# Kernel tuning notes

Measured on AMD Instinct MI355X. Metric: run time of the kernel, lower is better.

The kernel has to match this reference:

```python
import jax, jax.numpy as jnp
import numpy as np
from jax import lax

STRIDES = (8, 16, 32)
NUM_CLASSES = 80
TOPK = 1000
CONF_THRESH = 0.05
NMS_THRESH = 0.6


def setup_inputs() -> dict:
    key = jax.random.key(0)
    ks = jax.random.split(key, 10)
    hw = [(256, 256), (128, 128), (64, 64)]
    inp = {}
    for lv, (h, w) in enumerate(hw):
        inp[f"cls_pred_{lv}"] = jax.random.normal(ks[3 * lv + 0], (NUM_CLASSES, h, w), jnp.float32)
        inp[f"reg_pred_{lv}"] = jax.random.normal(ks[3 * lv + 1], (4, h, w), jnp.float32)
        inp[f"ctn_pred_{lv}"] = jax.random.normal(ks[3 * lv + 2], (1, h, w), jnp.float32)
    inp["scales"] = jax.random.uniform(ks[9], (3,), jnp.float32)
    return inp


def _level_decode(cls_p, reg_p, ctn_p, scale, stride):
    # cls_p: [C,H,W] -> flatten to [M,C] matching torch permute(1,2,0).view(-1,C)
    C, H, W = cls_p.shape
    cls = jnp.transpose(cls_p, (1, 2, 0)).reshape(-1, C)          # [M,C]
    reg = jnp.transpose(reg_p, (1, 2, 0)).reshape(-1, 4)          # [M,4]
    reg = jax.nn.relu(reg * scale) * stride                       # Scale + relu + stride
    ctn = jnp.transpose(ctn_p, (1, 2, 0)).reshape(-1, 1)          # [M,1]
    joint = jnp.sqrt(jax.nn.sigmooid(cls) * jax.nn.sigmoid(ctn)) if False else \
        jnp.sqrt(jax.nn.sigmoid(cls) * jax.nn.sigmoid(ctn))      # [M,C]
    scores = jnp.max(joint, axis=-1)                              # [M]
    labels = jnp.argmax(joint, axis=-1)                           # [M]
    ay, ax = jnp.meshgrid(jnp.arange(H), jnp.arange(W), indexing='ij')
    anchors = (jnp.stack([ax, ay], -1).reshape(-1, 2).astype(cls.dtype) + 0.5) * stride  # [M,2]
    # per-level topk (M > TOPK for all levels here)
    scores, idx = lax.top_k(scores, TOPK)
    labels = labels[idx]
    reg = reg[idx]
    anchors = anchors[idx]
    boxes = jnp.concatenate([anchors - reg[:, :2], anchors + reg[:, 2:]], axis=-1)  # x1y1x2y2
    return scores, labels, boxes


def _nms(boxes, scores):
    # Faithful port of the pure-python NMS: fixed-shape keep mask, sorted order.
    N = boxes.shape[0]
    order = jnp.argsort(-scores)
    b = boxes[order]
    x1, y1, x2, y2 = b[:, 0], b[:, 1], b[:, 2], b[:, 3]
    areas = (x2 - x1) * (y2 - y1)
    xx1 = jnp.maximum(x1[:, None], x1[None, :])
    yy1 = jnp.maximum(y1[:, None], y1[None, :])
    xx2 = jnp.minimum(x2[:, None], x2[None, :])
    yy2 = jnp.minimum(y2[:, None], y2[None, :])
    w = jnp.maximum(1e-10, xx2 - xx1)
    h = jnp.maximum(1e-10, yy2 - yy1)
    inter = w * h
    iou = inter / (areas[:, None] + areas[None, :] - inter + 1e-14)  # [N,N]
    idxs = jnp.arange(N)

    def body(i, keep):
        sup = (iou[i] > NMS_THRESH) & (idxs > i) & keep[i]
        return keep & ~sup

    keep = lax.fori_loop(0, N, body, jnp.ones((N,), bool))
    return order, keep


def reference(cls_pred_0, cls_pred_1, cls_pred_2,
              reg_pred_0, reg_pred_1, reg_pred_2,
              ctn_pred_0, ctn_pred_1, ctn_pred_2, scales):
    cls_l = [cls_pred_0, cls_pred_1, cls_pred_2]
    reg_l = [reg_pred_0, reg_pred_1, reg_pred_2]
    ctn_l = [ctn_pred_0, ctn_pred_1, ctn_pred_2]
    all_s, all_l, all_b = [], [], []
    for lv in range(3):
        s, lb, bx = _level_decode(cls_l[lv], reg_l[lv], ctn_l[lv], scales[lv], float(STRIDES[lv]))
        all_s.append(s); all_l.append(lb); all_b.append(bx)
    scores = jnp.concatenate(all_s)   # [3000]
    labels = jnp.concatenate(all_l)
    boxes = jnp.concatenate(all_b)    # [3000,4]
    order, keep = _nms(boxes, scores)
    scores_s = scores[order]
    labels_s = labels[order]
    boxes_s = boxes[order]
    keep = keep & (scores_s > CONF_THRESH)
    return boxes_s, scores_s, labels_s, keep
```

## Files before the change

kernel.cpp:

```cpp
#include <hip/hip_runtime.h>
#include <cmath>
#include <stdint.h>

#define NPTS   86016
#define NB     (1 << 18)
#define NCB    1024
#define K_TOP  1000
#define NOUT   3000
#define NWORDS 47
#define NTILE  47
#define CAND_CAP 16384
#define ECAP   8192
#define FCAP   1024
#define SPPB   64

#define HIST_OFF   0
#define CH_OFF     (NB * 3 * 4)
#define CNT_OFF    (CH_OFF + NCB * 3 * 4)
#define MEMSET_BYTES (CNT_OFF + 64)
#define KEYS_OFF   (CNT_OFF + 64)
#define LAB_OFF    (KEYS_OFF + NPTS * 8)
#define SURE_OFF   (LAB_OFF + NPTS * 4)
#define CAND_OFF   (SURE_OFF + 3 * 1024 * 8)
#define SURV_OFF   (CAND_OFF + 3 * CAND_CAP * 8)
#define EDGE_OFF   (SURV_OFF + NOUT * 8 + 64)
#define FLAG_OFF   (EDGE_OFF + ECAP * 4)

__device__ __forceinline__ float sig_f32_stepwise(float x) {
    float e = (float)exp(-(double)x);
    return 1.0f / (1.0f + e);
}

__device__ __forceinline__ void locate(int g, int& lv, int& p, int& HW) {
    if (g < 65536)      { lv = 0; p = g;         HW = 65536; }
    else if (g < 81920) { lv = 1; p = g - 65536; HW = 16384; }
    else                { lv = 2; p = g - 81920; HW = 4096;  }
}

__global__ __launch_bounds__(256) void score_kernel(
        const float* __restrict__ cls0, const float* __restrict__ cls1,
        const float* __restrict__ cls2,
        const float* __restrict__ ctn0, const float* __restrict__ ctn1,
        const float* __restrict__ ctn2,
        unsigned long long* __restrict__ keys, int* __restrict__ labels,
        int* __restrict__ hist, int* __restrict__ chist,
        int* __restrict__ cnt, unsigned* __restrict__ flags) {
    __shared__ float pm[5 * SPPB], pv[5 * SPPB];
    __shared__ int pidx[5 * SPPB];
    __shared__ int lch[NCB];
    const int tid = threadIdx.x;
    const int base = blockIdx.x * SPPB;
    for (int i = tid; i < NCB; i += 256) lch[i] = 0;
    for (int it = tid; it < 5 * SPPB; it += 256) {
        int c = it / SPPB, pt = it - c * SPPB;
        int g = base + pt, lv, p, HW;
        locate(g, lv, p, HW);
        const float* cls = (lv == 0) ? cls0 : ((lv == 1) ? cls1 : cls2);
        const float* bp = cls + (size_t)c * 16 * HW + p;
        float x[16];
#pragma unroll
        for (int cc = 0; cc < 16; cc++) x[cc] = bp[(size_t)cc * HW];
        float m = -INFINITY, v = -INFINITY; int idx = 0;
#pragma unroll
        for (int cc = 0; cc < 16; cc++)
            if (x[cc] > m) { v = m; m = x[cc]; idx = c * 16 + cc; }
        pm[it] = m; pv[it] = v; pidx[it] = idx;
    }
    __syncthreads();
    if (tid < SPPB) {
        int g = base + tid, lv, p, HW;
        locate(g, lv, p, HW);
        const float* ctn = (lv == 0) ? ctn0 : ((lv == 1) ? ctn1 : ctn2);
        float m = -INFINITY, v = -INFINITY; int idx = 0;
#pragma unroll
        for (int k = 0; k < 5; k++) {
            float bm = pm[k * SPPB + tid];
            float bv = pv[k * SPPB + tid];
            int bidx = pidx[k * SPPB + tid];
            if (bm > m) { v = fmaxf(m, bv); m = bm; idx = bidx; }
        }
        float sc = sig_f32_stepwise(ctn[p]);
        float sM = sig_f32_stepwise(m);
        float jm = __fsqrt_rn(sM * sc);
        float sV = sig_f32_stepwise(v);
        float jv = __fsqrt_rn(sV * sc);
        if (jv == jm) {
            int f = atomicAdd(&cnt[13], 1);
            if (f < FCAP) flags[f] = (unsigned)g;
        }
        unsigned int bits = __float_as_uint(jm);
        keys[g] = ((unsigned long long)bits << 32) | (0xFFFFFFFFu - (unsigned)g);
        labels[g] = idx;
        atomicAdd(&hist[lv * NB + (int)(bits >> 12)], 1);
        atomicAdd(&lch[(int)(bits >> 20)], 1);
    }
    __syncthreads();
    int lv0, p0, HW0; locate(base, lv0, p0, HW0);
    for (int i = tid; i < NCB; i += 256) {
        int v = lch[i];
        if (v) atomicAdd(&chist[lv0 * NCB + i], v);
    }
}

__global__ __launch_bounds__(1024) void thresh_kernel(
        const float* __restrict__ cls0, const float* __restrict__ cls1,
        const float* __restrict__ cls2,
        const float* __restrict__ ctn0, const float* __restrict__ ctn1,
        const float* __restrict__ ctn2,
        const int* __restrict__ hist, const int* __restrict__ chist,
        int* __restrict__ cnt,
        const unsigned* __restrict__ flags, int* __restrict__ labels) {
    int bid = blockIdx.x, tid = threadIdx.x;
    if (bid < 3) {
        int lv = bid;
        const int* h = hist + lv * NB;
        __shared__ int part[1024];
        __shared__ int s_chunk, s_above;
        __shared__ int bins[257];
        part[tid] = chist[lv * NCB + tid];
        __syncthreads();
        for (int off = 1; off < 1024; off <<= 1) {
            int v = part[tid] + ((tid + off < 1024) ? part[tid + off] : 0);
            __syncthreads(); part[tid] = v; __syncthreads();
        }
        int nxt = (tid < 1023) ? part[tid + 1] : 0;
        if (part[tid] >= K_TOP && nxt < K_TOP) { s_chunk = tid; s_above = nxt; }
        __syncthreads();
        int chunk = s_chunk, above = s_above;
        if (tid < 256) bins[tid] = h[chunk * 256 + tid];
        __syncthreads();
        for (int off = 1; off < 256; off <<= 1) {
            int v = 0;
            if (tid < 256) v = bins[tid] + ((tid + off < 256) ? bins[tid + off] : 0);
            __syncthreads(); if (tid < 256) bins[tid] = v; __syncthreads();
        }
        if (tid < 256) {
            int ge    = above + bins[tid];
            int genxt = above + ((tid < 255) ? bins[tid + 1] : 0);
            if (ge >= K_TOP && genxt < K_TOP) {
                cnt[6 + lv] = chunk * 256 + tid;
                cnt[9 + lv] = K_TOP - genxt;
            }
        }
    } else {
        int nf = cnt[13]; if (nf > FCAP) nf = FCAP;
        int wave = tid >> 6, lane = tid & 63;
        for (int f = wave; f < nf; f += 16) {
            int g = (int)flags[f], lv, p, HW;
            locate(g, lv, p, HW);
            const float* cls = (lv == 0) ? cls0 : ((lv == 1) ? cls1 : cls2);
            const float* ctn = (lv == 0) ? ctn0 : ((lv == 1) ? ctn1 : ctn2);
            float sc = sig_f32_stepwise(ctn[p]);
            float bestv = -1.0f; int besti = 127;
            {
                float s = sig_f32_stepwise(cls[(size_t)lane * HW + p]);
                float sj = __fsqrt_rn(s * sc);
                bestv = sj; besti = lane;
            }
            if (lane < 16) {
                int c2 = lane + 64;
                float s = sig_f32_stepwise(cls[(size_t)c2 * HW + p]);
                float sj = __fsqrt_rn(s * sc);
                if (sj > bestv) { bestv = sj; besti = c2; }
            }
            for (int off = 32; off; off >>= 1) {
                float ov = __shfl_xor(bestv, off, 64);
                int   oi = __shfl_xor(besti, off, 64);
                if (ov > bestv || (ov == bestv && oi < besti)) { bestv = ov; besti = oi; }
            }
            if (lane == 0) labels[g] = besti;
        }
    }
}

__global__ void compact_kernel(const unsigned long long* __restrict__ keys,
                               int* __restrict__ cnt,
                               unsigned long long* __restrict__ sure,
                               unsigned long long* __restrict__ cand) {
    int g = blockIdx.x * blockDim.x + threadIdx.x;
    if (g >= NPTS) return;
    int lv = (g < 65536) ? 0 : (g < 81920 ? 1 : 2);
    unsigned long long key = keys[g];
    int bin = (int)(key >> 44);
    int B = cnt[6 + lv];
    if (bin > B) {
        int i = atomicAdd(&cnt[0 + lv], 1);
        sure[lv * 1024 + i] = key;
    } else if (bin == B) {
        int i = atomicAdd(&cnt[3 + lv], 1);
        if (i < CAND_CAP) cand[lv * CAND_CAP + i] = key;
    }
}

__global__ void select_kernel(const int* __restrict__ cnt,
                              const unsigned long long* __restrict__ sure,
                              unsigned long long* __restrict__ cand,
                              unsigned long long* __restrict__ surv) {
    int lv = blockIdx.x, tid = threadIdx.x;
    unsigned long long* c = cand + lv * CAND_CAP;
    int n = cnt[3 + lv]; if (n > CAND_CAP) n = CAND_CAP;
    int R = cnt[9 + lv];
    int Ca = K_TOP - R;
    int m = 1; while (m < n) m <<= 1;
    for (int t = n + tid; t < m; t += 1024) c[t] = 0ULL;
    __syncthreads();
    for (int k = 2; k <= m; k <<= 1)
        for (int j = k >> 1; j > 0; j >>= 1) {
            for (int t = tid; t < m; t += 1024) {
                int l = t ^ j;
                if (l > t) {
                    unsigned long long a = c[t], b = c[l];
                    if (((t & k) == 0) ? (a < b) : (a > b)) { c[t] = b; c[l] = a; }
                }
            }
            __syncthreads();
        }
    __shared__ unsigned long long s[1024];
    s[tid] = (tid < Ca) ? sure[lv * 1024 + tid]
                        : ((tid < K_TOP) ? c[tid - Ca] : 0ULL);
    __syncthreads();
    for (int k = 2; k <= 1024; k <<= 1)
        for (int j = k >> 1; j > 0; j >>= 1) {
            int l = tid ^ j;
            if (l > tid) {
                unsigned long long a = s[tid], b = s[l];
                if (((tid & k) == 0) ? (a < b) : (a > b)) { s[tid] = b; s[l] = a; }
            }
            __syncthreads();
        }
    if (tid < K_TOP) surv[lv * K_TOP + tid] = s[tid];
}

__global__ __launch_bounds__(1024) void merge_emit_kernel(
        const unsigned long long* __restrict__ surv,
        const int* __restrict__ labels,
        const float* __restrict__ reg0, const float* __restrict__ reg1,
        const float* __restrict__ reg2,
        const float* __restrict__ scales,
        float* __restrict__ out) {
    __shared__ unsigned long long L[3][1024];
    __shared__ unsigned long long s[NOUT];
    int tid = threadIdx.x;
#pragma unroll
    for (int lv = 0; lv < 3; lv++)
        L[lv][tid] = (tid < K_TOP) ? surv[lv * K_TOP + tid] : 0ULL;
    __syncthreads();
    for (int e = tid; e < NOUT; e += 1024) {
        int a = e / K_TOP, i = e - a * K_TOP;
        unsigned long long key = L[a][i];
        int rank = i;
#pragma unroll
        for (int b = 0; b < 3; b++) {
            if (b == a) continue;
            int lo = 0, hi = K_TOP;
            while (lo < hi) {
                int mid = (lo + hi) >> 1;
                if (L[b][mid] > key) lo = mid + 1; else hi = mid;
            }
            rank += lo;
        }
        s[rank] = key;
    }
    __syncthreads();
    for (int r = tid; r < NOUT; r += 1024) {
        unsigned long long key = s[r];
        unsigned int bits = (unsigned)(key >> 32);
        float score = __uint_as_float(bits);
        unsigned int g = 0xFFFFFFFFu - (unsigned)(key & 0xFFFFFFFFULL);
        int lv, p;
        if (g < 65536u)      { lv = 0; p = (int)g; }
        else if (g < 81920u) { lv = 1; p = (int)g - 65536; }
        else                 { lv = 2; p = (int)g - 81920; }
        const float* rp = (lv == 0) ? reg0 : ((lv == 1) ? reg1 : reg2);
        int HW = (lv == 0) ? 65536 : ((lv == 1) ? 16384 : 4096);
        int W = 256 >> lv;
        float strideF = (float)(8 << lv);
        float scale = scales[lv];
        int x = p & (W - 1);
        int y = p >> (8 - lv);
        float r0 = fmaxf(0.0f, rp[0 * HW + p] * scale) * strideF;
        float r1 = fmaxf(0.0f, rp[1 * HW + p] * scale) * strideF;
        float r2 = fmaxf(0.0f, rp[2 * HW + p] * scale) * strideF;
        float r3 = fmaxf(0.0f, rp[3 * HW + p] * scale) * strideF;
        float ax = ((float)x + 0.5f) * strideF;
        float ay = ((float)y + 0.5f) * strideF;
        out[r * 4 + 0] = ax - r0;
        out[r * 4 + 1] = ay - r1;
        out[r * 4 + 2] = ax + r2;
        out[r * 4 + 3] = ay + r3;
        out[12000 + r] = score;
        out[15000 + r] = (float)labels[g];
    }
}

__global__ __launch_bounds__(256) void edge_kernel(const float* __restrict__ out,
                                                   unsigned* __restrict__ edges_g,
                                                   int* __restrict__ cnt) {
    __shared__ float x1[128], y1[128], x2[128], y2[128];
    int t = blockIdx.x, tid = threadIdx.x;
    int ta = 0, rem = t;
    while (rem >= NTILE - ta) { rem -= NTILE - ta; ta++; }
    int tb = ta + rem;
    if (tid < 64) {
        int gi = ta * 64 + tid;
        if (gi < NOUT) {
            float4 b = ((const float4*)out)[gi];
            x1[tid] = b.x; y1[tid] = b.y; x2[tid] = b.z; y2[tid] = b.w;
        }
    } else if (tid < 128) {
        int gj = tb * 64 + (tid - 64);
        if (gj < NOUT) {
            float4 b = ((const float4*)out)[gj];
            x1[tid] = b.x; y1[tid] = b.y; x2[tid] = b.z; y2[tid] = b.w;
        }
    }
    __syncthreads();
#pragma unroll
    for (int q = 0; q < 16; q++) {
        int idx = q * 256 + tid;
        int ii = idx >> 6, jj = idx & 63;
        int i = ta * 64 + ii, j = tb * 64 + jj;
        if (i < j && j < NOUT) {
            float ai = (x2[ii] - x1[ii]) * (y2[ii] - y1[ii]);
            float aj = (x2[64 + jj] - x1[64 + jj]) * (y2[64 + jj] - y1[64 + jj]);
            float xx1 = fmaxf(x1[ii], x1[64 + jj]), yy1 = fmaxf(y1[ii], y1[64 + jj]);
            float xx2 = fminf(x2[ii], x2[64 + jj]), yy2 = fminf(y2[ii], y2[64 + jj]);
            float ww = fmaxf(1e-10f, xx2 - xx1);
            float hh = fmaxf(1e-10f, yy2 - yy1);
            float inter = ww * hh;
            float iou = inter / (((ai + aj) - inter) + 1e-14f);
            if ((double)iou > 0.6) {
                int e = atomicAdd(&cnt[12], 1);
                if (e < ECAP) edges_g[e] = ((unsigned)i << 12) | (unsigned)j;
            }
        }
    }
}

__global__ __launch_bounds__(1024) void nms_sparse_kernel(
        const unsigned* __restrict__ edges_g,
        const int* __restrict__ cnt,
        const float* __restrict__ scores_s,
        float* __restrict__ keep_out) {
    __shared__ unsigned ed[ECAP];
    __shared__ unsigned long long supLds[NWORDS];
    int tid = threadIdx.x;
    int E = cnt[12]; if (E > ECAP) E = ECAP;
    int m = 1; while (m < E) m <<= 1;
    for (int t = tid; t < m; t += 1024) ed[t] = (t < E) ? edges_g[t] : 0xFFFFFFFFu;
    __syncthreads();
    for (int k = 2; k <= m; k <<= 1)
        for (int j = k >> 1; j > 0; j >>= 1) {
            for (int t = tid; t < m; t += 1024) {
                int l = t ^ j;
                if (l > t) {
                    unsigned a = ed[t], b = ed[l];
                    if (((t & k) == 0) ? (a > b) : (a < b)) { ed[t] = b; ed[l] = a; }
                }
            }
            __syncthreads();
        }
    if (tid < 64) {
        int lane = tid;
        unsigned long long supW = 0ULL;
        int ep = 0;
        for (int c = 0; c < NWORDS; c++) {
            unsigned long long cw = __shfl(supW, c, 64);
            int hi = (c + 1) * 64;
            while (ep < E) {
                unsigned k = ed[ep];
                int i = (int)(k >> 12);
                if (i >= hi) break;
                int j = (int)(k & 4095);
                if (!((cw >> (i & 63)) & 1ULL)) {
                    if ((j >> 6) == c) cw |= 1ULL << (j & 63);
                    else if (lane == (j >> 6)) supW |= 1ULL << (j & 63);
                }
                ep++;
            }
            if (lane == c) supW = cw;
        }
        if (lane < NWORDS) supLds[lane] = supW;
    }
    __syncthreads();
    for (int j = tid; j < NOUT; j += 1024) {
        bool s = (supLds[j >> 6] >> (j & 63)) & 1ULL;
        float scv = scores_s[j];
        keep_out[j] = (!s && ((double)scv > 0.05)) ? 1.0f : 0.0f;
    }
}

extern "C" void kernel_launch(void* const* d_in, const int* in_sizes, int n_in,
                              void* d_out, int out_size, void* d_ws, size_t ws_size,
                              hipStream_t stream) {
    const float* cls0 = (const float*)d_in[0];
    const float* reg0 = (const float*)d_in[1];
    const float* ctn0 = (const float*)d_in[2];
    const float* cls1 = (const float*)d_in[3];
    const float* reg1 = (const float*)d_in[4];
    const float* ctn1 = (const float*)d_in[5];
    const float* cls2 = (const float*)d_in[6];
    const float* reg2 = (const float*)d_in[7];
    const float* ctn2 = (const float*)d_in[8];
    const float* scales = (const float*)d_in[9];

    char* ws = (char*)d_ws;
    int* hist = (int*)(ws + HIST_OFF);
    int* chist = (int*)(ws + CH_OFF);
    int* cnt  = (int*)(ws + CNT_OFF);
    unsigned long long* keys = (unsigned long long*)(ws + KEYS_OFF);
    int* labels = (int*)(ws + LAB_OFF);
    unsigned long long* sure = (unsigned long long*)(ws + SURE_OFF);
    unsigned long long* cand = (unsigned long long*)(ws + CAND_OFF);
    unsigned long long* surv = (unsigned long long*)(ws + SURV_OFF);
    unsigned* edges = (unsigned*)(ws + EDGE_OFF);
    unsigned* flags = (unsigned*)(ws + FLAG_OFF);
    float* out = (float*)d_out;

    hipMemsetAsync(ws, 0, MEMSET_BYTES, stream);

    score_kernel<<<NPTS / SPPB, 256, 0, stream>>>(cls0, cls1, cls2, ctn0, ctn1, ctn2,
                                                  keys, labels, hist, chist, cnt, flags);
    thresh_kernel<<<4, 1024, 0, stream>>>(cls0, cls1, cls2, ctn0, ctn1, ctn2,
                                          hist, chist, cnt, flags, labels);
    compact_kernel<<<(NPTS + 255) / 256, 256, 0, stream>>>(keys, cnt, sure, cand);
    select_kernel<<<3, 1024, 0, stream>>>(cnt, sure, cand, surv);
    merge_emit_kernel<<<1, 1024, 0, stream>>>(surv, labels, reg0, reg1, reg2, scales, out);
    edge_kernel<<<NTILE * (NTILE + 1) / 2, 256, 0, stream>>>(out, edges, cnt);
    nms_sparse_kernel<<<1, 1024, 0, stream>>>(edges, cnt, out + 12000, out + 18000);
}
```

Before: 194.6 us.

## Fuse all FCOS post-processing stages into one cooperative persistent kernel

Replaces the memset plus seven separate kernel launches with a single cooperative kernel that runs every stage in turn, separated by grid-wide syncs, and zeroes the workspace in-kernel. The aim is to remove per-launch overhead and inter-kernel gaps, which matter because several stages are tiny single-block steps. In exchange, the scoring pass runs on a grid limited by occupancy, and the serial single-block phases (select, merge, NMS) now use 256 threads instead of 1024. Grid syncs also cost time, and the old multi-kernel path is kept as a fallback if the cooperative launch fails.

```diff
diff --git a/kernel.cpp b/kernel.cpp
--- a/kernel.cpp
+++ b/kernel.cpp
@@ -1,6 +1,9 @@
 #include <hip/hip_runtime.h>
+#include <hip/hip_cooperative_groups.h>
 #include <cmath>
 #include <stdint.h>
+
+namespace cg = cooperative_groups;
 
 #define NPTS   86016
 #define NB     (1 << 18)
@@ -9,10 +12,12 @@
 #define NOUT   3000
 #define NWORDS 47
 #define NTILE  47
+#define NTILES (NTILE * (NTILE + 1) / 2)
 #define CAND_CAP 16384
 #define ECAP   8192
 #define FCAP   1024
 #define SPPB   64
+#define NCHUNK (NPTS / SPPB)
 
 #define HIST_OFF   0
 #define CH_OFF     (NB * 3 * 4)
@@ -25,6 +30,7 @@
 #define SURV_OFF   (CAND_OFF + 3 * CAND_CAP * 8)
 #define EDGE_OFF   (SURV_OFF + NOUT * 8 + 64)
 #define FLAG_OFF   (EDGE_OFF + ECAP * 4)
+#define SMERGE_OFF (FLAG_OFF + FCAP * 4)
 
 __device__ __forceinline__ float sig_f32_stepwise(float x) {
     float e = (float)exp(-(double)x);
@@ -35,6 +41,373 @@
     if (g < 65536)      { lv = 0; p = g;         HW = 65536; }
     else if (g < 81920) { lv = 1; p = g - 65536; HW = 16384; }
     else                { lv = 2; p = g - 81920; HW = 4096;  }
+}
+
+__global__ __launch_bounds__(256, 4) void fcos_mega(
+        const float* __restrict__ cls0, const float* __restrict__ cls1,
+        const float* __restrict__ cls2,
+        const float* __restrict__ ctn0, const float* __restrict__ ctn1,
+        const float* __restrict__ ctn2,
+        const float* __restrict__ reg0, const float* __restrict__ reg1,
+        const float* __restrict__ reg2,
+        const float* __restrict__ scales, char* ws, float* out) {
+    cg::grid_group grid = cg::this_grid();
+    const int tid = threadIdx.x;
+    const int bid = blockIdx.x;
+    const int nblk = gridDim.x;
+
+    int* hist = (int*)(ws + HIST_OFF);
+    int* chist = (int*)(ws + CH_OFF);
+    int* cnt = (int*)(ws + CNT_OFF);
+    unsigned long long* keys = (unsigned long long*)(ws + KEYS_OFF);
+    int* labels = (int*)(ws + LAB_OFF);
+    unsigned long long* sure = (unsigned long long*)(ws + SURE_OFF);
+    unsigned long long* cand = (unsigned long long*)(ws + CAND_OFF);
+    unsigned long long* surv = (unsigned long long*)(ws + SURV_OFF);
+    unsigned* edges_g = (unsigned*)(ws + EDGE_OFF);
+    unsigned* flags = (unsigned*)(ws + FLAG_OFF);
+    unsigned long long* smerge = (unsigned long long*)(ws + SMERGE_OFF);
+
+    __shared__ union {
+        struct { float pm[5 * SPPB]; float pv[5 * SPPB]; int pidx[5 * SPPB]; int lch[NCB]; } sc;
+        struct { int part[1024]; int bins[257]; int s_chunk; int s_above; } th;
+        struct { unsigned long long s[1024]; } sel;
+        struct { unsigned long long L[3][1024]; } mg;
+        struct { float x1[128], y1[128], x2[128], y2[128]; } eg;
+        struct { unsigned ed[ECAP]; unsigned long long supLds[NWORDS]; } nm;
+    } sh;
+
+    {
+        int* w4 = (int*)ws;
+        const int tot = MEMSET_BYTES / 4;
+        for (int i = bid * 256 + tid; i < tot; i += nblk * 256) w4[i] = 0;
+    }
+    grid.sync();
+
+    for (int ch = bid; ch < NCHUNK; ch += nblk) {
+        const int base = ch * SPPB;
+        __syncthreads();
+        for (int i = tid; i < NCB; i += 256) sh.sc.lch[i] = 0;
+        for (int it = tid; it < 5 * SPPB; it += 256) {
+            int c = it / SPPB, pt = it - c * SPPB;
+            int g = base + pt, lv, p, HW;
+            locate(g, lv, p, HW);
+            const float* cls = (lv == 0) ? cls0 : ((lv == 1) ? cls1 : cls2);
+            const float* bp = cls + (size_t)c * 16 * HW + p;
+            float x[16];
+#pragma unroll
+            for (int cc = 0; cc < 16; cc++) x[cc] = bp[(size_t)cc * HW];
+            float m = -INFINITY, v = -INFINITY; int idx = 0;
+#pragma unroll
+            for (int cc = 0; cc < 16; cc++)
+                if (x[cc] > m) { v = m; m = x[cc]; idx = c * 16 + cc; }
+            sh.sc.pm[it] = m; sh.sc.pv[it] = v; sh.sc.pidx[it] = idx;
+        }
+        __syncthreads();
+        if (tid < SPPB) {
+            int g = base + tid, lv, p, HW;
+            locate(g, lv, p, HW);
+            const float* ctn = (lv == 0) ? ctn0 : ((lv == 1) ? ctn1 : ctn2);
+            float m = -INFINITY, v = -INFINITY; int idx = 0;
+#pragma unroll
+            for (int k = 0; k < 5; k++) {
+                float bm = sh.sc.pm[k * SPPB + tid];
+                float bv = sh.sc.pv[k * SPPB + tid];
+                int bidx = sh.sc.pidx[k * SPPB + tid];
+                if (bm > m) { v = fmaxf(m, bv); m = bm; idx = bidx; }
+            }
+            float sc = sig_f32_stepwise(ctn[p]);
+            float sM = sig_f32_stepwise(m);
+            float jm = __fsqrt_rn(sM * sc);
+            float sV = sig_f32_stepwise(v);
+            float jv = __fsqrt_rn(sV * sc);
+            if (jv == jm) {
+                int f = atomicAdd(&cnt[13], 1);
+                if (f < FCAP) flags[f] = (unsigned)g;
+            }
+            unsigned int bits = __float_as_uint(jm);
+            keys[g] = ((unsigned long long)bits << 32) | (0xFFFFFFFFu - (unsigned)g);
+            labels[g] = idx;
+            atomicAdd(&hist[lv * NB + (int)(bits >> 12)], 1);
+            atomicAdd(&sh.sc.lch[(int)(bits >> 20)], 1);
+        }
+        __syncthreads();
+        int lv0, p0, HW0; locate(base, lv0, p0, HW0);
+        for (int i = tid; i < NCB; i += 256) {
+            int v = sh.sc.lch[i];
+            if (v) atomicAdd(&chist[lv0 * NCB + i], v);
+        }
+    }
+    grid.sync();
+
+    if (bid < 3) {
+        int lv = bid;
+        const int* h = hist + lv * NB;
+#pragma unroll
+        for (int k = 0; k < 4; k++) sh.th.part[tid + k * 256] = chist[lv * NCB + tid + k * 256];
+        __syncthreads();
+        for (int off = 1; off < 1024; off <<= 1) {
+            int v[4];
+#pragma unroll
+            for (int k = 0; k < 4; k++) {
+                int i = tid + k * 256;
+                v[k] = sh.th.part[i] + ((i + off < 1024) ? sh.th.part[i + off] : 0);
+            }
+            __syncthreads();
+#pragma unroll
+            for (int k = 0; k < 4; k++) sh.th.part[tid + k * 256] = v[k];
+            __syncthreads();
+        }
+#pragma unroll
+        for (int k = 0; k < 4; k++) {
+            int i = tid + k * 256;
+            int nxt = (i < 1023) ? sh.th.part[i + 1] : 0;
+            if (sh.th.part[i] >= K_TOP && nxt < K_TOP) { sh.th.s_chunk = i; sh.th.s_above = nxt; }
+        }
+        __syncthreads();
+        int chunk = sh.th.s_chunk, above = sh.th.s_above;
+        sh.th.bins[tid] = h[chunk * 256 + tid];
+        __syncthreads();
+        for (int off = 1; off < 256; off <<= 1) {
+            int v = sh.th.bins[tid] + ((tid + off < 256) ? sh.th.bins[tid + off] : 0);
+            __syncthreads(); sh.th.bins[tid] = v; __syncthreads();
+        }
+        {
+            int ge    = above + sh.th.bins[tid];
+            int genxt = above + ((tid < 255) ? sh.th.bins[tid + 1] : 0);
+            if (ge >= K_TOP && genxt < K_TOP) {
+                cnt[6 + lv] = chunk * 256 + tid;
+                cnt[9 + lv] = K_TOP - genxt;
+            }
+        }
+    } else if (bid == 3) {
+        int nf = cnt[13]; if (nf > FCAP) nf = FCAP;
+        int wave = tid >> 6, lane = tid & 63;
+        for (int f = wave; f < nf; f += 4) {
+            int g = (int)flags[f], lv, p, HW;
+            locate(g, lv, p, HW);
+            const float* cls = (lv == 0) ? cls0 : ((lv == 1) ? cls1 : cls2);
+            const float* ctn = (lv == 0) ? ctn0 : ((lv == 1) ? ctn1 : ctn2);
+            float sc = sig_f32_stepwise(ctn[p]);
+            float bestv = -1.0f; int besti = 127;
+            {
+                float s = sig_f32_stepwise(cls[(size_t)lane * HW + p]);
+                float sj = __fsqrt_rn(s * sc);
+                bestv = sj; besti = lane;
+            }
+            if (lane < 16) {
+                int c2 = lane + 64;
+                float s = sig_f32_stepwise(cls[(size_t)c2 * HW + p]);
+                float sj = __fsqrt_rn(s * sc);
+                if (sj > bestv) { bestv = sj; besti = c2; }
+            }
+            for (int off = 32; off; off >>= 1) {
+                float ov = __shfl_xor(bestv, off, 64);
+                int   oi = __shfl_xor(besti, off, 64);
+                if (ov > bestv || (ov == bestv && oi < besti)) { bestv = ov; besti = oi; }
+            }
+            if (lane == 0) labels[g] = besti;
+        }
+    }
+    grid.sync();
+
+    for (int g = bid * 256 + tid; g < NPTS; g += nblk * 256) {
+        int lv = (g < 65536) ? 0 : (g < 81920 ? 1 : 2);
+        unsigned long long key = keys[g];
+        int bin = (int)(key >> 44);
+        int B = cnt[6 + lv];
+        if (bin > B) {
+            int i = atomicAdd(&cnt[0 + lv], 1);
+            sure[lv * 1024 + i] = key;
+        } else if (bin == B) {
+            int i = atomicAdd(&cnt[3 + lv], 1);
+            if (i < CAND_CAP) cand[lv * CAND_CAP + i] = key;
+        }
+    }
+    grid.sync();
+
+    if (bid < 3) {
+        int lv = bid;
+        unsigned long long* c = cand + lv * CAND_CAP;
+        int n = cnt[3 + lv]; if (n > CAND_CAP) n = CAND_CAP;
+        int R = cnt[9 + lv];
+        int Ca = K_TOP - R;
+        int m = 1; while (m < n) m <<= 1;
+        for (int t = n + tid; t < m; t += 256) c[t] = 0ULL;
+        __syncthreads();
+        for (int k = 2; k <= m; k <<= 1)
+            for (int j = k >> 1; j > 0; j >>= 1) {
+                for (int t = tid; t < m; t += 256) {
+                    int l = t ^ j;
+                    if (l > t) {
+                        unsigned long long a = c[t], b = c[l];
+                        if (((t & k) == 0) ? (a < b) : (a > b)) { c[t] = b; c[l] = a; }
+                    }
+                }
+                __syncthreads();
+            }
+        for (int i = tid; i < 1024; i += 256)
+            sh.sel.s[i] = (i < Ca) ? sure[lv * 1024 + i]
+                                   : ((i < K_TOP) ? c[i - Ca] : 0ULL);
+        __syncthreads();
+        for (int k = 2; k <= 1024; k <<= 1)
+            for (int j = k >> 1; j > 0; j >>= 1) {
+                for (int i = tid; i < 1024; i += 256) {
+                    int l = i ^ j;
+                    if (l > i) {
+                        unsigned long long a = sh.sel.s[i], b = sh.sel.s[l];
+                        if (((i & k) == 0) ? (a < b) : (a > b)) { sh.sel.s[i] = b; sh.sel.s[l] = a; }
+                    }
+                }
+                __syncthreads();
+            }
+        for (int i = tid; i < K_TOP; i += 256) surv[lv * K_TOP + i] = sh.sel.s[i];
+    }
+    grid.sync();
+
+    if (bid == 0) {
+        for (int i = tid; i < 1024; i += 256) {
+#pragma unroll
+            for (int lv = 0; lv < 3; lv++)
+                sh.mg.L[lv][i] = (i < K_TOP) ? surv[lv * K_TOP + i] : 0ULL;
+        }
+        __syncthreads();
+        for (int e = tid; e < NOUT; e += 256) {
+            int a = e / K_TOP, i = e - a * K_TOP;
+            unsigned long long key = sh.mg.L[a][i];
+            int rank = i;
+#pragma unroll
+            for (int b = 0; b < 3; b++) {
+                if (b == a) continue;
+                int lo = 0, hi = K_TOP;
+                while (lo < hi) {
+                    int mid = (lo + hi) >> 1;
+                    if (sh.mg.L[b][mid] > key) lo = mid + 1; else hi = mid;
+                }
+                rank += lo;
+            }
+            smerge[rank] = key;
+        }
+        __syncthreads();
+        for (int r = tid; r < NOUT; r += 256) {
+            unsigned long long key = smerge[r];
+            unsigned int bits = (unsigned)(key >> 32);
+            float score = __uint_as_float(bits);
+            unsigned int g = 0xFFFFFFFFu - (unsigned)(key & 0xFFFFFFFFULL);
+            int lv, p;
+            if (g < 65536u)      { lv = 0; p = (int)g; }
+            else if (g < 81920u) { lv = 1; p = (int)g - 65536; }
+            else                 { lv = 2; p = (int)g - 81920; }
+            const float* rp = (lv == 0) ? reg0 : ((lv == 1) ? reg1 : reg2);
+            int HW = (lv == 0) ? 65536 : ((lv == 1) ? 16384 : 4096);
+            int W = 256 >> lv;
+            float strideF = (float)(8 << lv);
+            float scale = scales[lv];
+            int x = p & (W - 1);
+            int y = p >> (8 - lv);
+            float r0 = fmaxf(0.0f, rp[0 * HW + p] * scale) * strideF;
+            float r1 = fmaxf(0.0f, rp[1 * HW + p] * scale) * strideF;
+            float r2 = fmaxf(0.0f, rp[2 * HW + p] * scale) * strideF;
+            float r3 = fmaxf(0.0f, rp[3 * HW + p] * scale) * strideF;
+            float ax = ((float)x + 0.5f) * strideF;
+            float ay = ((float)y + 0.5f) * strideF;
+            out[r * 4 + 0] = ax - r0;
+            out[r * 4 + 1] = ay - r1;
+            out[r * 4 + 2] = ax + r2;
+            out[r * 4 + 3] = ay + r3;
+            out[12000 + r] = score;
+            out[15000 + r] = (float)labels[g];
+        }
+    }
+    grid.sync();
+
+    for (int t = bid; t < NTILES; t += nblk) {
+        int ta = 0, rem = t;
+        while (rem >= NTILE - ta) { rem -= NTILE - ta; ta++; }
+        int tb = ta + rem;
+        __syncthreads();
+        if (tid < 64) {
+            int gi = ta * 64 + tid;
+            if (gi < NOUT) {
+                float4 b = ((const float4*)out)[gi];
+                sh.eg.x1[tid] = b.x; sh.eg.y1[tid] = b.y; sh.eg.x2[tid] = b.z; sh.eg.y2[tid] = b.w;
+            }
+        } else if (tid < 128) {
+            int gj = tb * 64 + (tid - 64);
+            if (gj < NOUT) {
+                float4 b = ((const float4*)out)[gj];
+                sh.eg.x1[tid] = b.x; sh.eg.y1[tid] = b.y; sh.eg.x2[tid] = b.z; sh.eg.y2[tid] = b.w;
+            }
+        }
+        __syncthreads();
+#pragma unroll
+        for (int q = 0; q < 16; q++) {
+            int idx = q * 256 + tid;
+            int ii = idx >> 6, jj = idx & 63;
+            int i = ta * 64 + ii, j = tb * 64 + jj;
+            if (i < j && j < NOUT) {
+                float ai = (sh.eg.x2[ii] - sh.eg.x1[ii]) * (sh.eg.y2[ii] - sh.eg.y1[ii]);
+                float aj = (sh.eg.x2[64 + jj] - sh.eg.x1[64 + jj]) * (sh.eg.y2[64 + jj] - sh.eg.y1[64 + jj]);
+                float xx1 = fmaxf(sh.eg.x1[ii], sh.eg.x1[64 + jj]), yy1 = fmaxf(sh.eg.y1[ii], sh.eg.y1[64 + jj]);
+                float xx2 = fminf(sh.eg.x2[ii], sh.eg.x2[64 + jj]), yy2 = fminf(sh.eg.y2[ii], sh.eg.y2[64 + jj]);
+                float ww = fmaxf(1e-10f, xx2 - xx1);
+                float hh = fmaxf(1e-10f, yy2 - yy1);
+                float inter = ww * hh;
+                float iou = inter / (((ai + aj) - inter) + 1e-14f);
+                if ((double)iou > 0.6) {
+                    int e = atomicAdd(&cnt[12], 1);
+                    if (e < ECAP) edges_g[e] = ((unsigned)i << 12) | (unsigned)j;
+                }
+            }
+        }
+    }
+    grid.sync();
+
+    if (bid == 0) {
+        int E = cnt[12]; if (E > ECAP) E = ECAP;
+        int m = 1; while (m < E) m <<= 1;
+        for (int t = tid; t < m; t += 256) sh.nm.ed[t] = (t < E) ? edges_g[t] : 0xFFFFFFFFu;
+        __syncthreads();
+        for (int k = 2; k <= m; k <<= 1)
+            for (int j = k >> 1; j > 0; j >>= 1) {
+                for (int t = tid; t < m; t += 256) {
+                    int l = t ^ j;
+                    if (l > t) {
+                        unsigned a = sh.nm.ed[t], b = sh.nm.ed[l];
+                        if (((t & k) == 0) ? (a > b) : (a < b)) { sh.nm.ed[t] = b; sh.nm.ed[l] = a; }
+                    }
+                }
+                __syncthreads();
+            }
+        if (tid < 64) {
+            int lane = tid;
+            unsigned long long supW = 0ULL;
+            int ep = 0;
+            for (int c = 0; c < NWORDS; c++) {
+                unsigned long long cw = __shfl(supW, c, 64);
+                int hi = (c + 1) * 64;
+                while (ep < E) {
+                    unsigned kk = sh.nm.ed[ep];
+                    int i = (int)(kk >> 12);
+                    if (i >= hi) break;
+                    int j = (int)(kk & 4095);
+                    if (!((cw >> (i & 63)) & 1ULL)) {
+                        if ((j >> 6) == c) cw |= 1ULL << (j & 63);
+                        else if (lane == (j >> 6)) supW |= 1ULL << (j & 63);
+                    }
+                    ep++;
+                }
+                if (lane == c) supW = cw;
+            }
+            if (lane < NWORDS) sh.nm.supLds[lane] = supW;
+        }
+        __syncthreads();
+        for (int j = tid; j < NOUT; j += 256) {
+            bool s = (sh.nm.supLds[j >> 6] >> (j & 63)) & 1ULL;
+            float scv = out[12000 + j];
+            out[18000 + j] = (!s && ((double)scv > 0.05)) ? 1.0f : 0.0f;
+        }
+    }
 }
 
 __global__ __launch_bounds__(256) void score_kernel(
@@ -405,27 +778,43 @@
     const float* scales = (const float*)d_in[9];
 
     char* ws = (char*)d_ws;
-    int* hist = (int*)(ws + HIST_OFF);
-    int* chist = (int*)(ws + CH_OFF);
-    int* cnt  = (int*)(ws + CNT_OFF);
-    unsigned long long* keys = (unsigned long long*)(ws + KEYS_OFF);
-    int* labels = (int*)(ws + LAB_OFF);
-    unsigned long long* sure = (unsigned long long*)(ws + SURE_OFF);
-    unsigned long long* cand = (unsigned long long*)(ws + CAND_OFF);
-    unsigned long long* surv = (unsigned long long*)(ws + SURV_OFF);
-    unsigned* edges = (unsigned*)(ws + EDGE_OFF);
-    unsigned* flags = (unsigned*)(ws + FLAG_OFF);
     float* out = (float*)d_out;
 
-    hipMemsetAsync(ws, 0, MEMSET_BYTES, stream);
-
-    score_kernel<<<NPTS / SPPB, 256, 0, stream>>>(cls0, cls1, cls2, ctn0, ctn1, ctn2,
-                                                  keys, labels, hist, chist, cnt, flags);
-    thresh_kernel<<<4, 1024, 0, stream>>>(cls0, cls1, cls2, ctn0, ctn1, ctn2,
-                                          hist, chist, cnt, flags, labels);
-    compact_kernel<<<(NPTS + 255) / 256, 256, 0, stream>>>(keys, cnt, sure, cand);
-    select_kernel<<<3, 1024, 0, stream>>>(cnt, sure, cand, surv);
-    merge_emit_kernel<<<1, 1024, 0, stream>>>(surv, labels, reg0, reg1, reg2, scales, out);
-    edge_kernel<<<NTILE * (NTILE + 1) / 2, 256, 0, stream>>>(out, edges, cnt);
-    nms_sparse_kernel<<<1, 1024, 0, stream>>>(edges, cnt, out + 12000, out + 18000);
-}
+    int occ = 0;
+    if (hipOccupancyMaxActiveBlocksPerMultiprocessor(&occ, fcos_mega, 256, 0) != hipSuccess || occ < 1)
+        occ = 4;
+    int grid = occ * 256;
+    if (grid > NCHUNK) grid = NCHUNK;
+
+    void* args[] = { (void*)&cls0, (void*)&cls1, (void*)&cls2,
+                     (void*)&ctn0, (void*)&ctn1, (void*)&ctn2,
+                     (void*)&reg0, (void*)&reg1, (void*)&reg2,
+                     (void*)&scales, (void*)&ws, (void*)&out };
+    hipError_t err = hipLaunchCooperativeKernel((const void*)fcos_mega,
+                                                dim3(grid), dim3(256),
+                                                args, 0, stream);
+    if (err != hipSuccess) {
+        (void)hipGetLastError();
+        int* hist = (int*)(ws + HIST_OFF);
+        int* chist = (int*)(ws + CH_OFF);
+        int* cnt  = (int*)(ws + CNT_OFF);
+        unsigned long long* keys = (unsigned long long*)(ws + KEYS_OFF);
+        int* labels = (int*)(ws + LAB_OFF);
+        unsigned long long* sure = (unsigned long long*)(ws + SURE_OFF);
+        unsigned long long* cand = (unsigned long long*)(ws + CAND_OFF);
+        unsigned long long* surv = (unsigned long long*)(ws + SURV_OFF);
+        unsigned* edges = (unsigned*)(ws + EDGE_OFF);
+        unsigned* flags = (unsigned*)(ws + FLAG_OFF);
+
+        hipMemsetAsync(ws, 0, MEMSET_BYTES, stream);
+        score_kernel<<<NPTS / SPPB, 256, 0, stream>>>(cls0, cls1, cls2, ctn0, ctn1, ctn2,
+                                                      keys, labels, hist, chist, cnt, flags);
+        thresh_kernel<<<4, 1024, 0, stream>>>(cls0, cls1, cls2, ctn0, ctn1, ctn2,
+                                              hist, chist, cnt, flags, labels);
+        compact_kernel<<<(NPTS + 255) / 256, 256, 0, stream>>>(keys, cnt, sure, cand);
+        select_kernel<<<3, 1024, 0, stream>>>(cnt, sure, cand, surv);
+        merge_emit_kernel<<<1, 1024, 0, stream>>>(surv, labels, reg0, reg1, reg2, scales, out);
+        edge_kernel<<<NTILE * (NTILE + 1) / 2, 256, 0, stream>>>(out, edges, cnt);
+        nms_sparse_kernel<<<1, 1024, 0, stream>>>(edges, cnt, out + 12000, out + 18000);
+    }
+}
```

Result: slower. 574.8 us (+195.4%).
